# Performance work log

Measured on AMD Instinct MI355X. Metric: run time of the kernel, lower is better.

## Reference

```python
import jax, jax.numpy as jnp
import numpy as np

TOPK = 4  # constructor default topk=4


def setup_inputs() -> dict:
    key = jax.random.key(0)
    k_x, k_a, k_b, k_w, k_bias = jax.random.split(key, 5)
    b, s, h, j, a, r = 4, 2048, 2048, 2048, 64, 16
    x = jax.random.normal(k_x, (b, s, h), dtype=jnp.float32)
    A = jax.random.normal(k_a, (a, r, h), dtype=jnp.float32) * 0.02   # adapter down-proj bank
    B = jax.random.normal(k_b, (a, j, r), dtype=jnp.float32) * 0.02   # adapter up-proj bank
    W = jax.random.normal(k_w, (j, h), dtype=jnp.float32) * 0.02      # base Linear weight
    bias = jax.random.normal(k_bias, (j,), dtype=jnp.float32) * 0.02  # base Linear bias
    return {"x": x, "A": A, "B": B, "W": W, "bias": bias}


def reference(x, A, B, W, bias):
    # vecs: per-adapter low-rank projections of each token. [b,s,a,r]
    vecs = jnp.einsum('arh,bsh->bsar', A, x)
    # routing score = L2 norm over rank dim. [b,s,a]
    arrows = jnp.linalg.norm(vecs, axis=-1)
    # top-k adapters per token -> uniform 1/topk routing weights (scatter of a constant,
    # so no gradient flows through the routing weights, matching torch semantics).
    _, idx = jax.lax.top_k(arrows, TOPK)                     # [b,s,topk]
    routes = jax.nn.one_hot(idx, arrows.shape[-1], dtype=x.dtype).sum(-2) / TOPK  # [b,s,a]
    # weighted combine of selected adapter vecs. [b,s,r]
    v = jnp.einsum('bsa,bsar->bsr', routes, vecs)
    # delta = (routes-weighted B) applied to v; contract over a then r without
    # materializing the [b,s,j,r] intermediate. [b,s,j]
    delta = jnp.einsum('bsa,ajr,bsr->bsj', routes, B, v)
    base = jnp.einsum('bsh,jh->bsj', x, W) + bias
    return base + delta
```

## Files before the change

### kernel.cpp

```cpp
#include <hip/hip_runtime.h>
#include <hip/hip_bf16.h>
#include <stdint.h>

#define TOKENS 8192
#define H 2048
#define JDIM 2048
#define NADAPT 64
#define RANK 16
#define KG 1024
#define KTOT 3072
#define NT2 48

typedef __bf16 v8bf __attribute__((ext_vector_type(8)));
typedef float v4f __attribute__((ext_vector_type(4)));
typedef unsigned short us8 __attribute__((ext_vector_type(8)));
typedef unsigned short us4 __attribute__((ext_vector_type(4)));

__device__ __forceinline__ unsigned short f2bf(float f) {
  union { __bf16 b; unsigned short u; } c; c.b = (__bf16)f; return c.u;
}
__device__ __forceinline__ float bf2f(unsigned short u) {
  union { unsigned int u; float f; } c; c.u = ((unsigned int)u) << 16; return c.f;
}

__device__ __forceinline__ us8 pack8(float4 a, float4 b) {
  us8 r;
  r[0]=f2bf(a.x); r[1]=f2bf(a.y); r[2]=f2bf(a.z); r[3]=f2bf(a.w);
  r[4]=f2bf(b.x); r[5]=f2bf(b.y); r[6]=f2bf(b.z); r[7]=f2bf(b.w);
  return r;
}

__device__ __forceinline__ void split8(float4 a, float4 b, us8& h, us8& l) {
  float v[8] = {a.x, a.y, a.z, a.w, b.x, b.y, b.z, b.w};
  #pragma unroll
  for (int i = 0; i < 8; ++i) {
    h[i] = f2bf(v[i]);
    l[i] = f2bf(v[i] - bf2f(h[i]));
  }
}

__global__ void cast_x_split_kernel(const float* __restrict__ x,
                                    unsigned short* __restrict__ XG,
                                    unsigned short* __restrict__ XLO) {
  int idx = blockIdx.x * 256 + threadIdx.x;
  int row = idx >> 8;
  int cg  = idx & 255;
  const float4* s = (const float4*)(x + ((size_t)row << 11) + ((size_t)cg << 3));
  float4 a = s[0], b = s[1];
  us8 h, l;
  split8(a, b, h, l);
  *(us8*)(XG  + (size_t)row * KTOT + ((size_t)cg << 3)) = h;
  *(us8*)(XLO + (size_t)row * H    + ((size_t)cg << 3)) = l;
}

__global__ void cast_a_split_kernel(const float* __restrict__ A,
                                    unsigned short* __restrict__ Ahi,
                                    unsigned short* __restrict__ Alo) {
  int idx = blockIdx.x * 256 + threadIdx.x;
  int row = idx >> 8;
  int cg  = idx & 255;
  const float4* s = (const float4*)(A + ((size_t)row << 11) + ((size_t)cg << 3));
  float4 a = s[0], b = s[1];
  us8 h, l;
  split8(a, b, h, l);
  *(us8*)(Ahi + (size_t)row * H + ((size_t)cg << 3)) = h;
  *(us8*)(Alo + (size_t)row * H + ((size_t)cg << 3)) = l;
}

__global__ void cast2048_kernel(const float* __restrict__ src,
                                unsigned short* __restrict__ dst, int dstld) {
  int idx = blockIdx.x * 256 + threadIdx.x;
  int row = idx >> 8;
  int cg  = idx & 255;
  const float4* s = (const float4*)(src + ((size_t)row << 11) + ((size_t)cg << 3));
  float4 a = s[0], b = s[1];
  *(us8*)(dst + (size_t)row * dstld + ((size_t)cg << 3)) = pack8(a, b);
}

__global__ void cast_b_kernel(const float* __restrict__ Bsrc,
                              unsigned short* __restrict__ WB) {
  int idx = blockIdx.x * 256 + threadIdx.x;
  int a = idx >> 11, j = idx & 2047;
  const float4* s = (const float4*)(Bsrc + (((size_t)a << 11) + j) * RANK);
  float4 f0 = s[0], f1 = s[1], f2 = s[2], f3 = s[3];
  us8* d = (us8*)(WB + (size_t)j * KTOT + H + a * RANK);
  d[0] = pack8(f0, f1);
  d[1] = pack8(f2, f3);
}

__global__ void route_kernel(const float* __restrict__ vecs,
                             unsigned short* __restrict__ XG) {
  __shared__ float vsh[4][16];
  int wave = threadIdx.x >> 6, lane = threadIdx.x & 63;
  int t = blockIdx.x * 4 + wave;
  const float* vrow = vecs + (size_t)t * KG;
  const float4* vp = (const float4*)(vrow + lane * RANK);
  float4 q0 = vp[0], q1 = vp[1], q2 = vp[2], q3 = vp[3];
  float ss = q0.x*q0.x + q0.y*q0.y + q0.z*q0.z + q0.w*q0.w
           + q1.x*q1.x + q1.y*q1.y + q1.z*q1.z + q1.w*q1.w
           + q2.x*q2.x + q2.y*q2.y + q2.z*q2.z + q2.w*q2.w
           + q3.x*q3.x + q3.y*q3.y + q3.z*q3.z + q3.w*q3.w;
  float arr = ss;
  int sel[4];
  #pragma unroll
  for (int k = 0; k < 4; ++k) {
    float m = arr; int mi = lane;
    #pragma unroll
    for (int o = 32; o > 0; o >>= 1) {
      float om = __shfl_xor(m, o);
      int oi  = __shfl_xor(mi, o);
      if (om > m || (om == m && oi < mi)) { m = om; mi = oi; }
    }
    sel[k] = mi;
    if (lane == mi) arr = -3.0e38f;
  }
  if (lane < 16) {
    float s = vrow[sel[0]*RANK + lane] + vrow[sel[1]*RANK + lane]
            + vrow[sel[2]*RANK + lane] + vrow[sel[3]*RANK + lane];
    vsh[wave][lane] = 0.0625f * s;
  }
  __syncthreads();
  bool on = (lane == sel[0]) | (lane == sel[1]) | (lane == sel[2]) | (lane == sel[3]);
  us8 lo, hi;
  #pragma unroll
  for (int r = 0; r < 8; ++r) lo[r] = on ? f2bf(vsh[wave][r])     : (unsigned short)0;
  #pragma unroll
  for (int r = 0; r < 8; ++r) hi[r] = on ? f2bf(vsh[wave][r + 8]) : (unsigned short)0;
  us8* d = (us8*)(XG + (size_t)t * KTOT + H + lane * RANK);
  d[0] = lo; d[1] = hi;
}

__device__ __forceinline__ void gload_lds16(const void* gsrc, void* ldst) {
  __builtin_amdgcn_global_load_lds(
      (const __attribute__((address_space(1))) unsigned int*)gsrc,
      (__attribute__((address_space(3))) unsigned int*)ldst, 16, 0, 0);
}

__global__ __launch_bounds__(256, 2) void gemm1_kernel(
    const unsigned short* __restrict__ Xhi,
    const unsigned short* __restrict__ Xlo,
    const unsigned short* __restrict__ Ahi,
    const unsigned short* __restrict__ Alo,
    float* __restrict__ C) {
  __shared__ unsigned short AsH[128 * 32];
  __shared__ unsigned short AsL[128 * 32];
  __shared__ unsigned short BsH[128 * 32];
  __shared__ unsigned short BsL[128 * 32];
  const int tid = threadIdx.x;
  const int lane = tid & 63, wave = tid >> 6;
  const int wr = wave >> 1, wc = wave & 1;
  const int bm = blockIdx.x, bn = blockIdx.y;

  v4f acc[4][4];
  #pragma unroll
  for (int i = 0; i < 4; ++i)
    #pragma unroll
    for (int j = 0; j < 4; ++j)
      acc[i][j] = (v4f){0.f, 0.f, 0.f, 0.f};

  const unsigned short* XhiB = Xhi + (size_t)(bm * 128) * KTOT;
  const unsigned short* XloB = Xlo + (size_t)(bm * 128) * H;
  const unsigned short* AhiB = Ahi + (size_t)(bn * 128) * H;
  const unsigned short* AloB = Alo + (size_t)(bn * 128) * H;

  const int rA = lane & 15;
  const int kk = (lane >> 4) << 3;

  for (int k0 = 0; k0 < H; k0 += 32) {
    #pragma unroll
    for (int rnd = 0; rnd < 2; ++rnd) {
      int e = rnd * 256 + tid;
      int r = e >> 2, c8 = (e & 3) << 3;
      gload_lds16(XhiB + (size_t)r * KTOT + k0 + c8, (char*)AsH + (size_t)e * 16);
      gload_lds16(XloB + (size_t)r * H    + k0 + c8, (char*)AsL + (size_t)e * 16);
      gload_lds16(AhiB + (size_t)r * H    + k0 + c8, (char*)BsH + (size_t)e * 16);
      gload_lds16(AloB + (size_t)r * H    + k0 + c8, (char*)BsL + (size_t)e * 16);
    }
    __syncthreads();
    v8bf ah[4], al[4], bh[4], bl[4];
    #pragma unroll
    for (int i = 0; i < 4; ++i) {
      ah[i] = *(const v8bf*)&AsH[(wr * 64 + i * 16 + rA) * 32 + kk];
      al[i] = *(const v8bf*)&AsL[(wr * 64 + i * 16 + rA) * 32 + kk];
    }
    #pragma unroll
    for (int j = 0; j < 4; ++j) {
      bh[j] = *(const v8bf*)&BsH[(wc * 64 + j * 16 + rA) * 32 + kk];
      bl[j] = *(const v8bf*)&BsL[(wc * 64 + j * 16 + rA) * 32 + kk];
    }
    #pragma unroll
    for (int i = 0; i < 4; ++i)
      #pragma unroll
      for (int j = 0; j < 4; ++j) {
        acc[i][j] = __builtin_amdgcn_mfma_f32_16x16x32_bf16(ah[i], bh[j], acc[i][j], 0, 0, 0);
        acc[i][j] = __builtin_amdgcn_mfma_f32_16x16x32_bf16(ah[i], bl[j], acc[i][j], 0, 0, 0);
        acc[i][j] = __builtin_amdgcn_mfma_f32_16x16x32_bf16(al[i], bh[j], acc[i][j], 0, 0, 0);
      }
    __syncthreads();
  }

  const int rowbase = bm * 128 + wr * 64;
  const int colbase = bn * 128 + wc * 64;
  #pragma unroll
  for (int i = 0; i < 4; ++i) {
    int r0 = rowbase + i * 16 + ((lane >> 4) << 2);
    #pragma unroll
    for (int j = 0; j < 4; ++j) {
      int col = colbase + j * 16 + (lane & 15);
      #pragma unroll
      for (int q = 0; q < 4; ++q)
        C[(size_t)(r0 + q) * KG + col] = acc[i][j][q];
    }
  }
}

#define BAR() asm volatile("s_waitcnt lgkmcnt(0)\n\ts_barrier" ::: "memory")
#define VM8() asm volatile("s_waitcnt vmcnt(8)" ::: "memory")

#define STAGE(regionUS, panel, kelem) do {                                        \
  gload_lds16((panel) + aoff0 + (kelem), (char*)(regionUS) + tid * 16);           \
  gload_lds16((panel) + aoff1 + (kelem), (char*)(regionUS) + 8192 + tid * 16);    \
} while (0)

#define PHASE(mh, RAr, RBr, ISSUE, DOVM) do {                                     \
  if ((mh) == 0) {                                                                \
    _Pragma("unroll")                                                             \
    for (int j = 0; j < 4; ++j)                                                   \
      bfr[j] = *(const v8bf*)((const char*)(RBr) + bbyte + j * 1024);             \
  }                                                                               \
  _Pragma("unroll")                                                               \
  for (int i = 0; i < 4; ++i)                                                     \
    af[i] = *(const v8bf*)((const char*)(RAr) + abyte + ((mh)*4 + i) * 1024);     \
  ISSUE;                                                                          \
  BAR();                                                                          \
  __builtin_amdgcn_s_setprio(1);                                                  \
  _Pragma("unroll")                                                               \
  for (int i = 0; i < 4; ++i)                                                     \
    _Pragma("unroll")                                                             \
    for (int j = 0; j < 4; ++j)                                                   \
      acc[(mh)*4 + i][j] = __builtin_amdgcn_mfma_f32_16x16x32_bf16(               \
          af[i], bfr[j], acc[(mh)*4 + i][j], 0, 0, 0);                            \
  __builtin_amdgcn_s_setprio(0);                                                  \
  DOVM;                                                                           \
  BAR();                                                                          \
} while (0)

__global__ __launch_bounds__(512, 1) void gemm2_8ph_kernel(
    const unsigned short* __restrict__ Xg, const unsigned short* __restrict__ Wb,
    float* __restrict__ C, const float* __restrict__ bias) {
  __shared__ unsigned short lds[65536];
  const int tid = threadIdx.x;
  const int lane = tid & 63, wid = tid >> 6;
  const int wr = wid >> 2, wc = wid & 3;
  const int rA = lane & 15, grp = lane >> 4;
  const int grpx = (grp ^ (rA & 3)) << 4;

  const int bid = blockIdx.x;
  const int bn = bid & 7, bm = bid >> 3;

  const unsigned short* Ap = Xg + (size_t)(bm * 256) * KTOT;
  const unsigned short* Bp = Wb + (size_t)(bn * 256) * KTOT;

  const int srow = tid >> 2;
  const int scol = ((tid & 3) ^ ((tid >> 2) & 3)) << 3;
  const size_t aoff0 = (size_t)srow * KTOT + scol;
  const size_t aoff1 = (size_t)(srow + 128) * KTOT + scol;

  unsigned short* A0k0 = lds;
  unsigned short* A0k1 = lds + 8192;
  unsigned short* B0k0 = lds + 16384;
  unsigned short* B0k1 = lds + 24576;
  unsigned short* A1k0 = lds + 32768;
  unsigned short* A1k1 = lds + 40960;
  unsigned short* B1k0 = lds + 49152;
  unsigned short* B1k1 = lds + 57344;

  const int abyte = (wr * 128 + rA) * 64 + grpx;
  const int bbyte = (wc * 64 + rA) * 64 + grpx;

  v4f acc[8][4];
  #pragma unroll
  for (int i = 0; i < 8; ++i)
    #pragma unroll
    for (int j = 0; j < 4; ++j)
      acc[i][j] = (v4f){0.f, 0.f, 0.f, 0.f};
  v8bf af[4], bfr[4];

  STAGE(A0k0, Ap, 0);
  STAGE(B0k0, Bp, 0);
  STAGE(A0k1, Ap, 32);
  STAGE(B0k1, Bp, 32);
  STAGE(A1k0, Ap, 64);
  STAGE(B1k0, Bp, 64);
  VM8();
  BAR();

  #pragma unroll 1
  for (int t = 0; t < NT2; t += 2) {
    const int k1a = (t + 1) * 64 + 32;
    const int k0a = (t + 2 < NT2 ? t + 2 : NT2 - 1) * 64;
    const int k1b = (t + 2 < NT2 ? t + 2 : NT2 - 1) * 64 + 32;
    const int k0b = (t + 3 < NT2 ? t + 3 : NT2 - 1) * 64;
    PHASE(0, A0k0, B0k0, STAGE(A1k1, Ap, k1a), ((void)0));
    PHASE(1, A0k0, B0k0, STAGE(B1k1, Bp, k1a), VM8());
    PHASE(0, A0k1, B0k1, STAGE(A0k0, Ap, k0a), ((void)0));
    PHASE(1, A0k1, B0k1, STAGE(B0k0, Bp, k0a), VM8());
    PHASE(0, A1k0, B1k0, STAGE(A0k1, Ap, k1b), ((void)0));
    PHASE(1, A1k0, B1k0, STAGE(B0k1, Bp, k1b), VM8());
    PHASE(0, A1k1, B1k1, STAGE(A1k0, Ap, k0b), ((void)0));
    PHASE(1, A1k1, B1k1, STAGE(B1k0, Bp, k0b), VM8());
  }

  const int row0 = bm * 256 + wr * 128 + (grp << 2);
  const int col0 = bn * 256 + wc * 64 + rA;
  float bv[4];
  #pragma unroll
  for (int j = 0; j < 4; ++j) bv[j] = bias[col0 + j * 16];
  #pragma unroll
  for (int mi = 0; mi < 8; ++mi)
    #pragma unroll
    for (int j = 0; j < 4; ++j)
      #pragma unroll
      for (int q = 0; q < 4; ++q)
        C[(size_t)(row0 + mi * 16 + q) * JDIM + col0 + j * 16] = acc[mi][j][q] + bv[j];
}

extern "C" void kernel_launch(void* const* d_in, const int* in_sizes, int n_in,
                              void* d_out, int out_size, void* d_ws, size_t ws_size,
                              hipStream_t stream) {
  const float* x    = (const float*)d_in[0];
  const float* A    = (const float*)d_in[1];
  const float* Bb   = (const float*)d_in[2];
  const float* W    = (const float*)d_in[3];
  const float* bias = (const float*)d_in[4];
  float* out = (float*)d_out;

  char* ws = (char*)d_ws;
  unsigned short* XG  = (unsigned short*)ws;
  unsigned short* WB  = (unsigned short*)(ws + (size_t)48 * 1024 * 1024);
  unsigned short* Ahi = (unsigned short*)(ws + (size_t)60 * 1024 * 1024);
  unsigned short* Alo = (unsigned short*)(ws + (size_t)64 * 1024 * 1024);
  float* vecs         = (float*)d_out;
  unsigned short* XLO = (unsigned short*)((char*)d_out + (size_t)32 * 1024 * 1024);

  cast_x_split_kernel<<<TOKENS, 256, 0, stream>>>(x, XG, XLO);
  cast_a_split_kernel<<<KG / 1, 256, 0, stream>>>(A, Ahi, Alo);
  cast2048_kernel<<<JDIM, 256, 0, stream>>>(W, WB, KTOT);
  cast_b_kernel<<<512, 256, 0, stream>>>(Bb, WB);

  gemm1_kernel<<<dim3(TOKENS / 128, KG / 128), 256, 0, stream>>>(
      XG, XLO, Ahi, Alo, vecs);

  route_kernel<<<TOKENS / 4, 256, 0, stream>>>(vecs, XG);

  gemm2_8ph_kernel<<<256, 512, 0, stream>>>(XG, WB, out, bias);
}
```

Baseline: 246.3 us.

## Use single fp16 GEMM for routing, recompute near-tie tokens in split-bf16

Replaces the split-bf16 routing projection, which ran three MFMAs per product, with a single fp16 GEMM. Tokens whose 4th and 5th adapter norms differ by less than a fixed epsilon are flagged and collected with an atomic counter. Those tokens are recomputed at higher precision by a gathered regemm kernel and then re-routed. The gemm2 and new LDS swizzles are also changed. The risk is that the recompute list is capped at a fixed size and the epsilon is a heuristic, so routing could silently differ from the reference if more tokens are ambiguous or errors exceed the epsilon.

After: 279.2 us. 1.13x slower.

```diff
diff --git a/kernel.cpp b/kernel.cpp
--- a/kernel.cpp
+++ b/kernel.cpp
@@ -10,8 +10,11 @@
 #define KG 1024
 #define KTOT 3072
 #define NT2 48
+#define CAP 2048
+#define EPS 0.01f
 
 typedef __bf16 v8bf __attribute__((ext_vector_type(8)));
+typedef _Float16 v8hf __attribute__((ext_vector_type(8)));
 typedef float v4f __attribute__((ext_vector_type(4)));
 typedef unsigned short us8 __attribute__((ext_vector_type(8)));
 typedef unsigned short us4 __attribute__((ext_vector_type(4)));
@@ -30,41 +33,49 @@
   return r;
 }
 
-__device__ __forceinline__ void split8(float4 a, float4 b, us8& h, us8& l) {
-  float v[8] = {a.x, a.y, a.z, a.w, b.x, b.y, b.z, b.w};
-  #pragma unroll
-  for (int i = 0; i < 8; ++i) {
-    h[i] = f2bf(v[i]);
-    l[i] = f2bf(v[i] - bf2f(h[i]));
-  }
-}
-
-__global__ void cast_x_split_kernel(const float* __restrict__ x,
-                                    unsigned short* __restrict__ XG,
-                                    unsigned short* __restrict__ XLO) {
+__device__ __forceinline__ void split4(float4 v, us4& h, us4& l) {
+  h[0]=f2bf(v.x); l[0]=f2bf(v.x - bf2f(h[0]));
+  h[1]=f2bf(v.y); l[1]=f2bf(v.y - bf2f(h[1]));
+  h[2]=f2bf(v.z); l[2]=f2bf(v.z - bf2f(h[2]));
+  h[3]=f2bf(v.w); l[3]=f2bf(v.w - bf2f(h[3]));
+}
+
+__global__ void cast_x_kernel(const float* __restrict__ x,
+                              unsigned short* __restrict__ XG,
+                              _Float16* __restrict__ Xf) {
   int idx = blockIdx.x * 256 + threadIdx.x;
-  int row = idx >> 8;
-  int cg  = idx & 255;
+  int row = idx >> 8, cg = idx & 255;
   const float4* s = (const float4*)(x + ((size_t)row << 11) + ((size_t)cg << 3));
   float4 a = s[0], b = s[1];
-  us8 h, l;
-  split8(a, b, h, l);
-  *(us8*)(XG  + (size_t)row * KTOT + ((size_t)cg << 3)) = h;
-  *(us8*)(XLO + (size_t)row * H    + ((size_t)cg << 3)) = l;
-}
-
-__global__ void cast_a_split_kernel(const float* __restrict__ A,
-                                    unsigned short* __restrict__ Ahi,
-                                    unsigned short* __restrict__ Alo) {
+  float v[8] = {a.x, a.y, a.z, a.w, b.x, b.y, b.z, b.w};
+  us8 h; v8hf f;
+  #pragma unroll
+  for (int i = 0; i < 8; ++i) { h[i] = f2bf(v[i]); f[i] = (_Float16)v[i]; }
+  *(us8*)(XG + (size_t)row * KTOT + ((size_t)cg << 3)) = h;
+  *(v8hf*)(Xf + ((size_t)row << 11) + ((size_t)cg << 3)) = f;
+}
+
+__global__ void cast_a_kernel(const float* __restrict__ A,
+                              _Float16* __restrict__ Af,
+                              unsigned short* __restrict__ Ahi,
+                              unsigned short* __restrict__ Alo,
+                              int* __restrict__ cnt) {
+  if (blockIdx.x == 0 && threadIdx.x == 0) *cnt = 0;
   int idx = blockIdx.x * 256 + threadIdx.x;
-  int row = idx >> 8;
-  int cg  = idx & 255;
+  int row = idx >> 8, cg = idx & 255;
   const float4* s = (const float4*)(A + ((size_t)row << 11) + ((size_t)cg << 3));
   float4 a = s[0], b = s[1];
-  us8 h, l;
-  split8(a, b, h, l);
-  *(us8*)(Ahi + (size_t)row * H + ((size_t)cg << 3)) = h;
-  *(us8*)(Alo + (size_t)row * H + ((size_t)cg << 3)) = l;
+  us4 h0, l0, h1, l1;
+  split4(a, h0, l0);
+  split4(b, h1, l1);
+  v8hf f;
+  float v[8] = {a.x, a.y, a.z, a.w, b.x, b.y, b.z, b.w};
+  #pragma unroll
+  for (int i = 0; i < 8; ++i) f[i] = (_Float16)v[i];
+  size_t o = ((size_t)row << 11) + ((size_t)cg << 3);
+  *(v8hf*)(Af + o) = f;
+  *(us4*)(Ahi + o) = h0; *(us4*)(Ahi + o + 4) = h1;
+  *(us4*)(Alo + o) = l0; *(us4*)(Alo + o + 4) = l1;
 }
 
 __global__ void cast2048_kernel(const float* __restrict__ src,
@@ -89,7 +100,8 @@
 }
 
 __global__ void route_kernel(const float* __restrict__ vecs,
-                             unsigned short* __restrict__ XG) {
+                             unsigned short* __restrict__ XG,
+                             int* __restrict__ cnt, int* __restrict__ tokidx) {
   __shared__ float vsh[4][16];
   int wave = threadIdx.x >> 6, lane = threadIdx.x & 63;
   int t = blockIdx.x * 4 + wave;
@@ -102,8 +114,9 @@
            + q3.x*q3.x + q3.y*q3.y + q3.z*q3.z + q3.w*q3.w;
   float arr = ss;
   int sel[4];
-  #pragma unroll
-  for (int k = 0; k < 4; ++k) {
+  float v4 = 0.f, v5 = 0.f;
+  #pragma unroll
+  for (int k = 0; k < 5; ++k) {
     float m = arr; int mi = lane;
     #pragma unroll
     for (int o = 32; o > 0; o >>= 1) {
@@ -111,8 +124,17 @@
       int oi  = __shfl_xor(mi, o);
       if (om > m || (om == m && oi < mi)) { m = om; mi = oi; }
     }
-    sel[k] = mi;
-    if (lane == mi) arr = -3.0e38f;
+    if (k < 4) {
+      sel[k] = mi;
+      if (lane == mi) arr = -3.0e38f;
+    }
+    if (k == 3) v4 = m;
+    if (k == 4) v5 = m;
+  }
+  bool flag = (sqrtf(v4) - sqrtf(v5)) < EPS;
+  if (flag && lane == 0) {
+    int p = atomicAdd(cnt, 1);
+    if (p < CAP) tokidx[p] = t;
   }
   if (lane < 16) {
     float s = vrow[sel[0]*RANK + lane] + vrow[sel[1]*RANK + lane]
@@ -136,20 +158,93 @@
       (__attribute__((address_space(3))) unsigned int*)ldst, 16, 0, 0);
 }
 
-__global__ __launch_bounds__(256, 2) void gemm1_kernel(
-    const unsigned short* __restrict__ Xhi,
-    const unsigned short* __restrict__ Xlo,
-    const unsigned short* __restrict__ Ahi,
-    const unsigned short* __restrict__ Alo,
+__global__ __launch_bounds__(256, 2) void gemm1f16_kernel(
+    const _Float16* __restrict__ Xf, const _Float16* __restrict__ Af,
     float* __restrict__ C) {
+  __shared__ _Float16 As[128 * 32];
+  __shared__ _Float16 Bs[128 * 32];
+  const int tid = threadIdx.x;
+  const int lane = tid & 63, wave = tid >> 6;
+  const int wr = wave >> 1, wc = wave & 1;
+  const int bm = blockIdx.x, bn = blockIdx.y;
+
+  v4f acc[4][4];
+  #pragma unroll
+  for (int i = 0; i < 4; ++i)
+    #pragma unroll
+    for (int j = 0; j < 4; ++j)
+      acc[i][j] = (v4f){0.f, 0.f, 0.f, 0.f};
+
+  const _Float16* Abase = Xf + ((size_t)(bm * 128) << 11);
+  const _Float16* Bbase = Af + ((size_t)(bn * 128) << 11);
+
+  const int rA = lane & 15;
+  const int kkx = (((lane >> 4) ^ ((rA >> 1) & 3)) << 3);
+
+  for (int k0 = 0; k0 < H; k0 += 32) {
+    #pragma unroll
+    for (int rnd = 0; rnd < 2; ++rnd) {
+      int e = rnd * 256 + tid;
+      int r = e >> 2;
+      int c8 = (((e & 3) ^ ((e >> 3) & 3)) << 3);
+      gload_lds16(Abase + ((size_t)r << 11) + k0 + c8, (char*)As + (size_t)e * 16);
+      gload_lds16(Bbase + ((size_t)r << 11) + k0 + c8, (char*)Bs + (size_t)e * 16);
+    }
+    __syncthreads();
+    v8hf af[4], bfr[4];
+    #pragma unroll
+    for (int i = 0; i < 4; ++i)
+      af[i] = *(const v8hf*)&As[(wr * 64 + i * 16 + rA) * 32 + kkx];
+    #pragma unroll
+    for (int j = 0; j < 4; ++j)
+      bfr[j] = *(const v8hf*)&Bs[(wc * 64 + j * 16 + rA) * 32 + kkx];
+    #pragma unroll
+    for (int i = 0; i < 4; ++i)
+      #pragma unroll
+      for (int j = 0; j < 4; ++j)
+        acc[i][j] = __builtin_amdgcn_mfma_f32_16x16x32_f16(af[i], bfr[j], acc[i][j], 0, 0, 0);
+    __syncthreads();
+  }
+
+  const int rowbase = bm * 128 + wr * 64;
+  const int colbase = bn * 128 + wc * 64;
+  #pragma unroll
+  for (int i = 0; i < 4; ++i) {
+    int r0 = rowbase + i * 16 + ((lane >> 4) << 2);
+    #pragma unroll
+    for (int j = 0; j < 4; ++j) {
+      int col = colbase + j * 16 + (lane & 15);
+      #pragma unroll
+      for (int q = 0; q < 4; ++q)
+        C[(size_t)(r0 + q) * KG + col] = acc[i][j][q];
+    }
+  }
+}
+
+__global__ __launch_bounds__(256, 2) void regemm_kernel(
+    const float* __restrict__ x, const unsigned short* __restrict__ Ahi,
+    const unsigned short* __restrict__ Alo, float* __restrict__ vecs,
+    const int* __restrict__ cnt, const int* __restrict__ tokidx) {
+  int cn = *cnt; if (cn > CAP) cn = CAP;
+  const int mblk = blockIdx.x;
+  if (mblk * 128 >= cn) return;
+
   __shared__ unsigned short AsH[128 * 32];
   __shared__ unsigned short AsL[128 * 32];
   __shared__ unsigned short BsH[128 * 32];
   __shared__ unsigned short BsL[128 * 32];
+  __shared__ int toks[128];
+
   const int tid = threadIdx.x;
+  if (tid < 128) {
+    int m = mblk * 128 + tid;
+    toks[tid] = (m < cn) ? tokidx[m] : tokidx[0];
+  }
+  __syncthreads();
+
   const int lane = tid & 63, wave = tid >> 6;
   const int wr = wave >> 1, wc = wave & 1;
-  const int bm = blockIdx.x, bn = blockIdx.y;
+  const int bn = blockIdx.y;
 
   v4f acc[4][4];
   #pragma unroll
@@ -158,23 +253,28 @@
     for (int j = 0; j < 4; ++j)
       acc[i][j] = (v4f){0.f, 0.f, 0.f, 0.f};
 
-  const unsigned short* XhiB = Xhi + (size_t)(bm * 128) * KTOT;
-  const unsigned short* XloB = Xlo + (size_t)(bm * 128) * H;
-  const unsigned short* AhiB = Ahi + (size_t)(bn * 128) * H;
-  const unsigned short* AloB = Alo + (size_t)(bn * 128) * H;
-
+  const unsigned short* AhiB = Ahi + ((size_t)(bn * 128) << 11);
+  const unsigned short* AloB = Alo + ((size_t)(bn * 128) << 11);
   const int rA = lane & 15;
   const int kk = (lane >> 4) << 3;
 
   for (int k0 = 0; k0 < H; k0 += 32) {
+    #pragma unroll
+    for (int rnd = 0; rnd < 4; ++rnd) {
+      int u = rnd * 256 + tid;
+      int r = u >> 3, c4 = (u & 7) << 2;
+      float4 xv = *(const float4*)(x + ((size_t)toks[r] << 11) + k0 + c4);
+      us4 xh, xl;
+      split4(xv, xh, xl);
+      *(us4*)&AsH[r * 32 + c4] = xh;
+      *(us4*)&AsL[r * 32 + c4] = xl;
+    }
     #pragma unroll
     for (int rnd = 0; rnd < 2; ++rnd) {
       int e = rnd * 256 + tid;
       int r = e >> 2, c8 = (e & 3) << 3;
-      gload_lds16(XhiB + (size_t)r * KTOT + k0 + c8, (char*)AsH + (size_t)e * 16);
-      gload_lds16(XloB + (size_t)r * H    + k0 + c8, (char*)AsL + (size_t)e * 16);
-      gload_lds16(AhiB + (size_t)r * H    + k0 + c8, (char*)BsH + (size_t)e * 16);
-      gload_lds16(AloB + (size_t)r * H    + k0 + c8, (char*)BsL + (size_t)e * 16);
+      gload_lds16(AhiB + ((size_t)r << 11) + k0 + c8, (char*)BsH + (size_t)e * 16);
+      gload_lds16(AloB + ((size_t)r << 11) + k0 + c8, (char*)BsL + (size_t)e * 16);
     }
     __syncthreads();
     v8bf ah[4], al[4], bh[4], bl[4];
@@ -199,19 +299,70 @@
     __syncthreads();
   }
 
-  const int rowbase = bm * 128 + wr * 64;
   const int colbase = bn * 128 + wc * 64;
   #pragma unroll
   for (int i = 0; i < 4; ++i) {
-    int r0 = rowbase + i * 16 + ((lane >> 4) << 2);
+    int lr0 = wr * 64 + i * 16 + ((lane >> 4) << 2);
     #pragma unroll
     for (int j = 0; j < 4; ++j) {
-      int col = colbase + j * 16 + (lane & 15);
+      int col = colbase + j * 16 + rA;
       #pragma unroll
-      for (int q = 0; q < 4; ++q)
-        C[(size_t)(r0 + q) * KG + col] = acc[i][j][q];
-    }
-  }
+      for (int q = 0; q < 4; ++q) {
+        int lr = lr0 + q;
+        if (mblk * 128 + lr < cn)
+          vecs[(size_t)toks[lr] * KG + col] = acc[i][j][q];
+      }
+    }
+  }
+}
+
+__global__ void route_fix_kernel(const float* __restrict__ vecs,
+                                 unsigned short* __restrict__ XG,
+                                 const int* __restrict__ cnt,
+                                 const int* __restrict__ tokidx) {
+  int cn = *cnt; if (cn > CAP) cn = CAP;
+  int i = blockIdx.x * 4 + (threadIdx.x >> 6);
+  if (i >= cn) return;
+  int lane = threadIdx.x & 63;
+  int t = tokidx[i];
+  const float* vrow = vecs + (size_t)t * KG;
+  const float4* vp = (const float4*)(vrow + lane * RANK);
+  float4 q0 = vp[0], q1 = vp[1], q2 = vp[2], q3 = vp[3];
+  float ss = q0.x*q0.x + q0.y*q0.y + q0.z*q0.z + q0.w*q0.w
+           + q1.x*q1.x + q1.y*q1.y + q1.z*q1.z + q1.w*q1.w
+           + q2.x*q2.x + q2.y*q2.y + q2.z*q2.z + q2.w*q2.w
+           + q3.x*q3.x + q3.y*q3.y + q3.z*q3.z + q3.w*q3.w;
+  float arr = ss;
+  int sel[4];
+  #pragma unroll
+  for (int k = 0; k < 4; ++k) {
+    float m = arr; int mi = lane;
+    #pragma unroll
+    for (int o = 32; o > 0; o >>= 1) {
+      float om = __shfl_xor(m, o);
+      int oi  = __shfl_xor(mi, o);
+      if (om > m || (om == m && oi < mi)) { m = om; mi = oi; }
+    }
+    sel[k] = mi;
+    if (lane == mi) arr = -3.0e38f;
+  }
+  int r = lane & 15;
+  float g = 0.0625f * (vrow[sel[0]*RANK + r] + vrow[sel[1]*RANK + r]
+                     + vrow[sel[2]*RANK + r] + vrow[sel[3]*RANK + r]);
+  bool on = (lane == sel[0]) | (lane == sel[1]) | (lane == sel[2]) | (lane == sel[3]);
+  us8 lo, hi;
+  #pragma unroll
+  for (int k = 0; k < 8; ++k) {
+    float gv = __shfl(g, k);
+    lo[k] = on ? f2bf(gv) : (unsigned short)0;
+  }
+  #pragma unroll
+  for (int k = 0; k < 8; ++k) {
+    float gv = __shfl(g, k + 8);
+    hi[k] = on ? f2bf(gv) : (unsigned short)0;
+  }
+  us8* d = (us8*)(XG + (size_t)t * KTOT + H + lane * RANK);
+  d[0] = lo; d[1] = hi;
 }
 
 #define BAR() asm volatile("s_waitcnt lgkmcnt(0)\n\ts_barrier" ::: "memory")
@@ -253,7 +404,7 @@
   const int lane = tid & 63, wid = tid >> 6;
   const int wr = wid >> 2, wc = wid & 3;
   const int rA = lane & 15, grp = lane >> 4;
-  const int grpx = (grp ^ (rA & 3)) << 4;
+  const int grpx = (grp ^ ((rA >> 1) & 3)) << 4;
 
   const int bid = blockIdx.x;
   const int bn = bid & 7, bm = bid >> 3;
@@ -262,7 +413,7 @@
   const unsigned short* Bp = Wb + (size_t)(bn * 256) * KTOT;
 
   const int srow = tid >> 2;
-  const int scol = ((tid & 3) ^ ((tid >> 2) & 3)) << 3;
+  const int scol = ((tid & 3) ^ ((tid >> 3) & 3)) << 3;
   const size_t aoff0 = (size_t)srow * KTOT + scol;
   const size_t aoff1 = (size_t)(srow + 128) * KTOT + scol;
 
@@ -340,18 +491,24 @@
   unsigned short* WB  = (unsigned short*)(ws + (size_t)48 * 1024 * 1024);
   unsigned short* Ahi = (unsigned short*)(ws + (size_t)60 * 1024 * 1024);
   unsigned short* Alo = (unsigned short*)(ws + (size_t)64 * 1024 * 1024);
+  _Float16* Af16      = (_Float16*)(ws + (size_t)68 * 1024 * 1024);
+  int* cnt            = (int*)(ws + (size_t)72 * 1024 * 1024);
+  int* tokidx         = cnt + 16;
   float* vecs         = (float*)d_out;
-  unsigned short* XLO = (unsigned short*)((char*)d_out + (size_t)32 * 1024 * 1024);
-
-  cast_x_split_kernel<<<TOKENS, 256, 0, stream>>>(x, XG, XLO);
-  cast_a_split_kernel<<<KG / 1, 256, 0, stream>>>(A, Ahi, Alo);
+  _Float16* Xf16      = (_Float16*)((char*)d_out + (size_t)32 * 1024 * 1024);
+
+  cast_x_kernel<<<TOKENS, 256, 0, stream>>>(x, XG, Xf16);
+  cast_a_kernel<<<KG, 256, 0, stream>>>(A, Af16, Ahi, Alo, cnt);
   cast2048_kernel<<<JDIM, 256, 0, stream>>>(W, WB, KTOT);
   cast_b_kernel<<<512, 256, 0, stream>>>(Bb, WB);
 
-  gemm1_kernel<<<dim3(TOKENS / 128, KG / 128), 256, 0, stream>>>(
-      XG, XLO, Ahi, Alo, vecs);
-
-  route_kernel<<<TOKENS / 4, 256, 0, stream>>>(vecs, XG);
+  gemm1f16_kernel<<<dim3(TOKENS / 128, KG / 128), 256, 0, stream>>>(Xf16, Af16, vecs);
+
+  route_kernel<<<TOKENS / 4, 256, 0, stream>>>(vecs, XG, cnt, tokidx);
+
+  regemm_kernel<<<dim3(CAP / 128, KG / 128), 256, 0, stream>>>(
+      x, Ahi, Alo, vecs, cnt, tokidx);
+  route_fix_kernel<<<CAP / 4, 256, 0, stream>>>(vecs, XG, cnt, tokidx);
 
   gemm2_8ph_kernel<<<256, 512, 0, stream>>>(XG, WB, out, bias);
 }
```
